# Performance work log

Hardware: AMD Instinct MI355X
Metric: run time of the kernel (lower is better)

The kernel has to match this reference:

```python
import jax, jax.numpy as jnp
import numpy as np

NUM_IN, NUM_OUT, SD, BATCH = 2048, 8192, 5, 4096
INIT_DELTA = 0.01


def _dist(a, b):
    # a: [I,1,D], b: [1,O,D] -> [I,O]
    return jnp.sqrt(jnp.sum((a - b) ** 2, axis=-1))


def setup_inputs() -> dict:
    key = jax.random.key(0)
    k1, k2, k3, k4, k5 = jax.random.split(key, 5)
    init_in_pos = jax.random.normal(k1, (NUM_IN, 1, SD), dtype=jnp.float32)
    init_out_pos = jax.random.normal(k2, (1, NUM_OUT, SD), dtype=jnp.float32)
    in_pos = init_in_pos + INIT_DELTA * jax.random.normal(k3, (NUM_IN, 1, SD), dtype=jnp.float32)
    out_pos = init_out_pos + INIT_DELTA * jax.random.normal(k4, (1, NUM_OUT, SD), dtype=jnp.float32)
    inputs = jax.random.normal(k5, (BATCH, NUM_IN), dtype=jnp.float32)
    biases = jnp.zeros((NUM_OUT,), dtype=jnp.float32)
    return {"inputs": inputs, "init_in_pos": init_in_pos, "init_out_pos": init_out_pos,
            "in_pos": in_pos, "out_pos": out_pos, "biases": biases}


def reference(inputs, init_in_pos, init_out_pos, in_pos, out_pos, biases):
    # weight = ||in_pos - out_pos|| - ||init_in_pos - init_out_pos||, shape [I,O]
    w = _dist(in_pos, out_pos) - _dist(init_in_pos, init_out_pos)
    return inputs @ w + biases
```

## Files before the change

kernel.cpp:

```cpp
#include <hip/hip_runtime.h>
#include <hip/hip_bf16.h>
#include <stdint.h>

#define NUM_IN  2048
#define NUM_OUT 8192
#define BATCH   4096
#define SD      5

#define BM 256
#define BN 256
#define BK 32
#define NT (NUM_IN / BK)
#define BUFE (BM * BK)

typedef __bf16 bf16x8 __attribute__((ext_vector_type(8)));
typedef float  f32x16 __attribute__((ext_vector_type(16)));
typedef unsigned short ushort_t;
typedef ushort_t ushort8 __attribute__((ext_vector_type(8)));

static __device__ __forceinline__ ushort_t bf16_bits(float f) {
  __hip_bfloat16 h = __float2bfloat16(f);
  ushort_t u;
  __builtin_memcpy(&u, &h, 2);
  return u;
}

__global__ __launch_bounds__(256) void cvt_kernel(const float* __restrict__ x,
                                                  ushort_t* __restrict__ y) {
  const int i = (blockIdx.x * 256 + threadIdx.x) * 8;
  float4 v0 = *reinterpret_cast<const float4*>(x + i);
  float4 v1 = *reinterpret_cast<const float4*>(x + i + 4);
  ushort8 o;
  o[0] = bf16_bits(v0.x); o[1] = bf16_bits(v0.y);
  o[2] = bf16_bits(v0.z); o[3] = bf16_bits(v0.w);
  o[4] = bf16_bits(v1.x); o[5] = bf16_bits(v1.y);
  o[6] = bf16_bits(v1.z); o[7] = bf16_bits(v1.w);
  *reinterpret_cast<ushort8*>(y + i) = o;
}

__global__ __launch_bounds__(256) void genw_kernel(
    const float* __restrict__ in_pos, const float* __restrict__ out_pos,
    const float* __restrict__ init_in, const float* __restrict__ init_out,
    ushort_t* __restrict__ Wt) {
  __shared__ float s_ip[NUM_IN * SD];
  __shared__ float s_iip[NUM_IN * SD];
  const int tid = threadIdx.x;
#pragma unroll
  for (int i = 0; i < 10; ++i) {
    const int idx = i * 1024 + tid * 4;
    *reinterpret_cast<float4*>(&s_ip[idx]) =
        *reinterpret_cast<const float4*>(in_pos + idx);
    *reinterpret_cast<float4*>(&s_iip[idx]) =
        *reinterpret_cast<const float4*>(init_in + idx);
  }
  __syncthreads();

  const int n  = blockIdx.x * 16 + (tid >> 4);
  const int kg = tid & 15;
  float op[SD], iop[SD];
#pragma unroll
  for (int d = 0; d < SD; ++d) {
    op[d]  = out_pos[n * SD + d];
    iop[d] = init_out[n * SD + d];
  }
#pragma unroll 1
  for (int kb = 0; kb < 16; ++kb) {
    const int k0 = kb * 128 + kg * 8;
    float buf[40], ibuf[40];
#pragma unroll
    for (int j = 0; j < 10; ++j) {
      float4 v = *reinterpret_cast<const float4*>(&s_ip[k0 * SD + j * 4]);
      buf[4 * j + 0] = v.x; buf[4 * j + 1] = v.y;
      buf[4 * j + 2] = v.z; buf[4 * j + 3] = v.w;
      float4 u = *reinterpret_cast<const float4*>(&s_iip[k0 * SD + j * 4]);
      ibuf[4 * j + 0] = u.x; ibuf[4 * j + 1] = u.y;
      ibuf[4 * j + 2] = u.z; ibuf[4 * j + 3] = u.w;
    }
    ushort8 o;
#pragma unroll
    for (int i = 0; i < 8; ++i) {
      float d1 = 0.f, d0 = 0.f;
#pragma unroll
      for (int d = 0; d < SD; ++d) {
        float a = buf[i * SD + d] - op[d];
        float b = ibuf[i * SD + d] - iop[d];
        d1 += a * a;
        d0 += b * b;
      }
      o[i] = bf16_bits(sqrtf(d1) - sqrtf(d0));
    }
    *reinterpret_cast<ushort8*>(Wt + (size_t)n * NUM_IN + k0) = o;
  }
}

__global__ __launch_bounds__(512, 2) void gemm_kernel(
    const ushort_t* __restrict__ A,
    const ushort_t* __restrict__ Bt,
    const float* __restrict__ bias,
    float* __restrict__ C) {
  __shared__ __align__(16) ushort_t sA[4 * BUFE];
  __shared__ __align__(16) ushort_t sB[4 * BUFE];

  const int tid = threadIdx.x;
  const int w   = tid >> 6;
  const int l   = tid & 63;
  const int wm  = w >> 2;
  const int wn  = w & 3;

  const int orig = blockIdx.x;
  const int lin  = (orig & 7) * 64 + (orig >> 3);
  const int bx   = lin >> 4;
  const int by   = lin & 15;
  const int m0   = by * BM;
  const int n0   = bx * BN;

  const int rl  = l & 31;
  const int hi  = l >> 5;
  const int le  = (l >> 1) & 7;
  const int p4  = (l & 1) * 4;
  const int phys0 = (p4 + 0 + hi) ^ le;
  const int phys1 = (p4 + 2 + hi) ^ le;
  const int lineoff = (rl >> 1) * 64;
  const int aoff0 = wm * 4096 + lineoff + phys0 * 8;
  const int aoff1 = wm * 4096 + lineoff + phys1 * 8;
  const int boff0 = wn * 2048 + lineoff + phys0 * 8;
  const int boff1 = wn * 2048 + lineoff + phys1 * 8;

  const int idx0 = tid, idx1 = tid + 512;
  const int c0 = (idx0 & 7) ^ ((idx0 >> 3) & 7);
  const int c1 = (idx1 & 7) ^ ((idx1 >> 3) & 7);
  const int row0 = 2 * (idx0 >> 3) + (c0 >> 2), k0e = (c0 & 3) * 8;
  const int row1 = 2 * (idx1 >> 3) + (c1 >> 2), k1e = (c1 & 3) * 8;
  const ushort_t* gA0 = A  + (size_t)(m0 + row0) * NUM_IN + k0e;
  const ushort_t* gA1 = A  + (size_t)(m0 + row1) * NUM_IN + k1e;
  const ushort_t* gB0 = Bt + (size_t)(n0 + row0) * NUM_IN + k0e;
  const ushort_t* gB1 = Bt + (size_t)(n0 + row1) * NUM_IN + k1e;

#define GLDS(src, dst)                                                         \
  __builtin_amdgcn_global_load_lds(                                            \
      reinterpret_cast<const __attribute__((address_space(1))) uint32_t*>(     \
          (uintptr_t)(src)),                                                   \
      reinterpret_cast<__attribute__((address_space(3))) uint32_t*>(           \
          (uintptr_t)(dst)),                                                   \
      16, 0, 0)

#define STAGE(bs, kt)                                                          \
  {                                                                            \
    GLDS(gA0 + (kt), &sA[(bs) * BUFE + idx0 * 8]);                             \
    GLDS(gA1 + (kt), &sA[(bs) * BUFE + idx1 * 8]);                             \
    GLDS(gB0 + (kt), &sB[(bs) * BUFE + idx0 * 8]);                             \
    GLDS(gB1 + (kt), &sB[(bs) * BUFE + idx1 * 8]);                             \
  }

  f32x16 acc[4][2];
#pragma unroll
  for (int i = 0; i < 4; ++i)
#pragma unroll
    for (int j = 0; j < 2; ++j)
#pragma unroll
      for (int r = 0; r < 16; ++r) acc[i][j][r] = 0.f;

  STAGE(0, 0)
  STAGE(1, BK)
  asm volatile("s_waitcnt vmcnt(4)" ::: "memory");
  __builtin_amdgcn_s_barrier();
  __builtin_amdgcn_sched_barrier(0);

#pragma unroll 1
  for (int t = 0; t < NT; ++t) {
    const int bufo = (t & 3) * BUFE;
    if (t < NT - 2) {
      STAGE((t + 2) & 3, (t + 2) * BK)
    }
    bf16x8 a[4][2], b[2][2];
#pragma unroll
    for (int mi = 0; mi < 4; ++mi) {
      a[mi][0] = *reinterpret_cast<const bf16x8*>(&sA[bufo + aoff0 + mi * 1024]);
      a[mi][1] = *reinterpret_cast<const bf16x8*>(&sA[bufo + aoff1 + mi * 1024]);
    }
#pragma unroll
    for (int ni = 0; ni < 2; ++ni) {
      b[ni][0] = *reinterpret_cast<const bf16x8*>(&sB[bufo + boff0 + ni * 1024]);
      b[ni][1] = *reinterpret_cast<const bf16x8*>(&sB[bufo + boff1 + ni * 1024]);
    }
    __builtin_amdgcn_s_setprio(1);
#pragma unroll
    for (int mi = 0; mi < 4; ++mi)
#pragma unroll
      for (int ni = 0; ni < 2; ++ni) {
        acc[mi][ni] = __builtin_amdgcn_mfma_f32_32x32x16_bf16(
            a[mi][0], b[ni][0], acc[mi][ni], 0, 0, 0);
        acc[mi][ni] = __builtin_amdgcn_mfma_f32_32x32x16_bf16(
            a[mi][1], b[ni][1], acc[mi][ni], 0, 0, 0);
      }
    __builtin_amdgcn_s_setprio(0);
    if (t < NT - 2) {
      asm volatile("s_waitcnt vmcnt(4)" ::: "memory");
    } else {
      asm volatile("s_waitcnt vmcnt(0)" ::: "memory");
    }
    __builtin_amdgcn_s_barrier();
    __builtin_amdgcn_sched_barrier(0);
  }

  const int crow = m0 + wm * 128 + 4 * hi;
  const int ccol = n0 + wn * 64 + rl;
#pragma unroll
  for (int ni = 0; ni < 2; ++ni) {
    const float bi = bias[ccol + ni * 32];
#pragma unroll
    for (int mi = 0; mi < 4; ++mi) {
#pragma unroll
      for (int reg = 0; reg < 16; ++reg) {
        const int r = crow + mi * 32 + (reg & 3) + 8 * (reg >> 2);
        C[(size_t)r * NUM_OUT + ccol + ni * 32] = acc[mi][ni][reg] + bi;
      }
    }
  }
#undef STAGE
#undef GLDS
}

extern "C" void kernel_launch(void* const* d_in, const int* in_sizes, int n_in,
                              void* d_out, int out_size, void* d_ws, size_t ws_size,
                              hipStream_t stream) {
  const float* inputs   = (const float*)d_in[0];
  const float* init_in  = (const float*)d_in[1];
  const float* init_out = (const float*)d_in[2];
  const float* in_pos   = (const float*)d_in[3];
  const float* out_pos  = (const float*)d_in[4];
  const float* biases   = (const float*)d_in[5];
  float* out = (float*)d_out;

  ushort_t* Abf = (ushort_t*)d_ws;
  ushort_t* Wt  = (ushort_t*)((char*)d_ws + (size_t)BATCH * NUM_IN * 2);

  cvt_kernel<<<(BATCH * NUM_IN) / (256 * 8), 256, 0, stream>>>(inputs, Abf);
  genw_kernel<<<NUM_OUT / 16, 256, 0, stream>>>(
      in_pos, out_pos, init_in, init_out, Wt);
  gemm_kernel<<<(BATCH / BM) * (NUM_OUT / BN), 512, 0, stream>>>(
      Abf, Wt, biases, out);
}
```

Baseline: 185.3 us.

## Restructure GEMM into 8-phase ping-pong schedule with 16x16x32 MFMA and BK=64

Measured after the change: 165.8 us. 10.5% less time.

```diff
diff --git a/kernel.cpp b/kernel.cpp
--- a/kernel.cpp
+++ b/kernel.cpp
@@ -9,12 +9,13 @@
 
 #define BM 256
 #define BN 256
-#define BK 32
+#define BK 64
 #define NT (NUM_IN / BK)
-#define BUFE (BM * BK)
+#define NI (NT / 2)
+#define TILEE (BM * BK)
 
 typedef __bf16 bf16x8 __attribute__((ext_vector_type(8)));
-typedef float  f32x16 __attribute__((ext_vector_type(16)));
+typedef float  f32x4  __attribute__((ext_vector_type(4)));
 typedef unsigned short ushort_t;
 typedef ushort_t ushort8 __attribute__((ext_vector_type(8)));
 
@@ -93,19 +94,21 @@
   }
 }
 
-__global__ __launch_bounds__(512, 2) void gemm_kernel(
+__global__ __launch_bounds__(512, 1) void gemm_kernel(
     const ushort_t* __restrict__ A,
     const ushort_t* __restrict__ Bt,
     const float* __restrict__ bias,
     float* __restrict__ C) {
-  __shared__ __align__(16) ushort_t sA[4 * BUFE];
-  __shared__ __align__(16) ushort_t sB[4 * BUFE];
-
-  const int tid = threadIdx.x;
-  const int w   = tid >> 6;
-  const int l   = tid & 63;
-  const int wm  = w >> 2;
-  const int wn  = w & 3;
+  __shared__ __align__(16) ushort_t sA[2 * TILEE];
+  __shared__ __align__(16) ushort_t sB[2 * TILEE];
+
+  const int tid  = threadIdx.x;
+  const int w    = tid >> 6;
+  const int l    = tid & 63;
+  const int wm   = w >> 2;
+  const int wn   = w & 3;
+  const int lrow = l & 15;
+  const int lkc  = l >> 4;
 
   const int orig = blockIdx.x;
   const int lin  = (orig & 7) * 64 + (orig >> 3);
@@ -114,27 +117,19 @@
   const int m0   = by * BM;
   const int n0   = bx * BN;
 
-  const int rl  = l & 31;
-  const int hi  = l >> 5;
-  const int le  = (l >> 1) & 7;
-  const int p4  = (l & 1) * 4;
-  const int phys0 = (p4 + 0 + hi) ^ le;
-  const int phys1 = (p4 + 2 + hi) ^ le;
-  const int lineoff = (rl >> 1) * 64;
-  const int aoff0 = wm * 4096 + lineoff + phys0 * 8;
-  const int aoff1 = wm * 4096 + lineoff + phys1 * 8;
-  const int boff0 = wn * 2048 + lineoff + phys0 * 8;
-  const int boff1 = wn * 2048 + lineoff + phys1 * 8;
-
-  const int idx0 = tid, idx1 = tid + 512;
-  const int c0 = (idx0 & 7) ^ ((idx0 >> 3) & 7);
-  const int c1 = (idx1 & 7) ^ ((idx1 >> 3) & 7);
-  const int row0 = 2 * (idx0 >> 3) + (c0 >> 2), k0e = (c0 & 3) * 8;
-  const int row1 = 2 * (idx1 >> 3) + (c1 >> 2), k1e = (c1 & 3) * 8;
-  const ushort_t* gA0 = A  + (size_t)(m0 + row0) * NUM_IN + k0e;
-  const ushort_t* gA1 = A  + (size_t)(m0 + row1) * NUM_IN + k1e;
-  const ushort_t* gB0 = Bt + (size_t)(n0 + row0) * NUM_IN + k0e;
-  const ushort_t* gB1 = Bt + (size_t)(n0 + row1) * NUM_IN + k1e;
+  const int ck0 = (lkc ^ (lrow & 7)) * 8;
+  const int ck1 = ((4 + lkc) ^ (lrow & 7)) * 8;
+  const int Ab  = wm * 4096 + lrow * 64;
+  const int Bb  = wn * 2048 + lrow * 64;
+
+  const int d0 = tid, d1 = tid + 512;
+  const int lr0 = d0 >> 3, lr1 = d1 >> 3;
+  const int c0 = (d0 & 7) ^ (lr0 & 7);
+  const int c1 = (d1 & 7) ^ (lr1 & 7);
+  const ushort_t* pA0 = A  + (size_t)(m0 + (lr0 >> 6) * 128 + (lr0 & 63)) * NUM_IN + c0 * 8;
+  const ushort_t* pA1 = A  + (size_t)(m0 + (lr1 >> 6) * 128 + (lr1 & 63)) * NUM_IN + c1 * 8;
+  const ushort_t* pB0 = Bt + (size_t)(n0 + (lr0 >> 5) * 64 + (lr0 & 31)) * NUM_IN + c0 * 8;
+  const ushort_t* pB1 = Bt + (size_t)(n0 + (lr1 >> 5) * 64 + (lr1 & 31)) * NUM_IN + c1 * 8;
 
 #define GLDS(src, dst)                                                         \
   __builtin_amdgcn_global_load_lds(                                            \
@@ -144,80 +139,162 @@
           (uintptr_t)(dst)),                                                   \
       16, 0, 0)
 
-#define STAGE(bs, kt)                                                          \
-  {                                                                            \
-    GLDS(gA0 + (kt), &sA[(bs) * BUFE + idx0 * 8]);                             \
-    GLDS(gA1 + (kt), &sA[(bs) * BUFE + idx1 * 8]);                             \
-    GLDS(gB0 + (kt), &sB[(bs) * BUFE + idx0 * 8]);                             \
-    GLDS(gB1 + (kt), &sB[(bs) * BUFE + idx1 * 8]);                             \
-  }
-
-  f32x16 acc[4][2];
-#pragma unroll
-  for (int i = 0; i < 4; ++i)
-#pragma unroll
-    for (int j = 0; j < 2; ++j)
-#pragma unroll
-      for (int r = 0; r < 16; ++r) acc[i][j][r] = 0.f;
-
-  STAGE(0, 0)
-  STAGE(1, BK)
-  asm volatile("s_waitcnt vmcnt(4)" ::: "memory");
-  __builtin_amdgcn_s_barrier();
-  __builtin_amdgcn_sched_barrier(0);
+#define STAGE_A(bs, mh, kt)                                                    \
+  {                                                                            \
+    GLDS(pA0 + (size_t)(mh) * 64 * NUM_IN + (kt),                              \
+         &sA[(bs) * TILEE + (mh) * 8192 + tid * 8]);                           \
+    GLDS(pA1 + (size_t)(mh) * 64 * NUM_IN + (kt),                              \
+         &sA[(bs) * TILEE + (mh) * 8192 + tid * 8 + 4096]);                    \
+  }
+#define STAGE_B(bs, nh, kt)                                                    \
+  {                                                                            \
+    GLDS(pB0 + (size_t)(nh) * 32 * NUM_IN + (kt),                              \
+         &sB[(bs) * TILEE + (nh) * 8192 + tid * 8]);                           \
+    GLDS(pB1 + (size_t)(nh) * 32 * NUM_IN + (kt),                              \
+         &sB[(bs) * TILEE + (nh) * 8192 + tid * 8 + 4096]);                    \
+  }
+
+#define RD_A(bs, mh)                                                           \
+  {                                                                            \
+    _Pragma("unroll")                                                          \
+    for (int mi = 0; mi < 4; ++mi) {                                           \
+      a[mi][0] = *reinterpret_cast<const bf16x8*>(                             \
+          &sA[(bs) * TILEE + (mh) * 8192 + Ab + mi * 1024 + ck0]);             \
+      a[mi][1] = *reinterpret_cast<const bf16x8*>(                             \
+          &sA[(bs) * TILEE + (mh) * 8192 + Ab + mi * 1024 + ck1]);             \
+    }                                                                          \
+  }
+#define RD_B(bs, nh, arr)                                                      \
+  {                                                                            \
+    _Pragma("unroll")                                                          \
+    for (int nj = 0; nj < 2; ++nj) {                                           \
+      arr[nj][0] = *reinterpret_cast<const bf16x8*>(                           \
+          &sB[(bs) * TILEE + (nh) * 8192 + Bb + nj * 1024 + ck0]);             \
+      arr[nj][1] = *reinterpret_cast<const bf16x8*>(                           \
+          &sB[(bs) * TILEE + (nh) * 8192 + Bb + nj * 1024 + ck1]);             \
+    }                                                                          \
+  }
+
+#define MFMA_Q(mh, nh, arr)                                                    \
+  {                                                                            \
+    __builtin_amdgcn_s_setprio(1);                                             \
+    _Pragma("unroll")                                                          \
+    for (int mi = 0; mi < 4; ++mi)                                             \
+      _Pragma("unroll")                                                        \
+      for (int nj = 0; nj < 2; ++nj) {                                         \
+        acc[(mh) * 4 + mi][(nh) * 2 + nj] =                                    \
+            __builtin_amdgcn_mfma_f32_16x16x32_bf16(                           \
+                a[mi][0], arr[nj][0], acc[(mh) * 4 + mi][(nh) * 2 + nj],       \
+                0, 0, 0);                                                      \
+        acc[(mh) * 4 + mi][(nh) * 2 + nj] =                                    \
+            __builtin_amdgcn_mfma_f32_16x16x32_bf16(                           \
+                a[mi][1], arr[nj][1], acc[(mh) * 4 + mi][(nh) * 2 + nj],       \
+                0, 0, 0);                                                      \
+      }                                                                        \
+    __builtin_amdgcn_s_setprio(0);                                             \
+  }
+
+#define BARRIER  __builtin_amdgcn_s_barrier()
+#define SCHED0   __builtin_amdgcn_sched_barrier(0)
+#define LGKM0    asm volatile("s_waitcnt lgkmcnt(0)" ::: "memory")
+#define VMCNT4   asm volatile("s_waitcnt vmcnt(4)" ::: "memory")
+
+  f32x4 acc[8][4];
+#pragma unroll
+  for (int i = 0; i < 8; ++i)
+#pragma unroll
+    for (int j = 0; j < 4; ++j) acc[i][j] = f32x4{0.f, 0.f, 0.f, 0.f};
+
+  STAGE_A(0, 0, 0) STAGE_B(0, 0, 0) STAGE_A(0, 1, 0) STAGE_B(0, 1, 0)
+  STAGE_A(1, 0, BK) STAGE_B(1, 0, BK)
+  VMCNT4;
+  BARRIER;
+  SCHED0;
 
 #pragma unroll 1
-  for (int t = 0; t < NT; ++t) {
-    const int bufo = (t & 3) * BUFE;
-    if (t < NT - 2) {
-      STAGE((t + 2) & 3, (t + 2) * BK)
-    }
-    bf16x8 a[4][2], b[2][2];
-#pragma unroll
-    for (int mi = 0; mi < 4; ++mi) {
-      a[mi][0] = *reinterpret_cast<const bf16x8*>(&sA[bufo + aoff0 + mi * 1024]);
-      a[mi][1] = *reinterpret_cast<const bf16x8*>(&sA[bufo + aoff1 + mi * 1024]);
-    }
-#pragma unroll
-    for (int ni = 0; ni < 2; ++ni) {
-      b[ni][0] = *reinterpret_cast<const bf16x8*>(&sB[bufo + boff0 + ni * 1024]);
-      b[ni][1] = *reinterpret_cast<const bf16x8*>(&sB[bufo + boff1 + ni * 1024]);
-    }
-    __builtin_amdgcn_s_setprio(1);
-#pragma unroll
-    for (int mi = 0; mi < 4; ++mi)
-#pragma unroll
-      for (int ni = 0; ni < 2; ++ni) {
-        acc[mi][ni] = __builtin_amdgcn_mfma_f32_32x32x16_bf16(
-            a[mi][0], b[ni][0], acc[mi][ni], 0, 0, 0);
-        acc[mi][ni] = __builtin_amdgcn_mfma_f32_32x32x16_bf16(
-            a[mi][1], b[ni][1], acc[mi][ni], 0, 0, 0);
-      }
-    __builtin_amdgcn_s_setprio(0);
-    if (t < NT - 2) {
-      asm volatile("s_waitcnt vmcnt(4)" ::: "memory");
-    } else {
-      asm volatile("s_waitcnt vmcnt(0)" ::: "memory");
-    }
-    __builtin_amdgcn_s_barrier();
-    __builtin_amdgcn_sched_barrier(0);
-  }
-
-  const int crow = m0 + wm * 128 + 4 * hi;
-  const int ccol = n0 + wn * 64 + rl;
-#pragma unroll
-  for (int ni = 0; ni < 2; ++ni) {
-    const float bi = bias[ccol + ni * 32];
-#pragma unroll
-    for (int mi = 0; mi < 4; ++mi) {
-#pragma unroll
-      for (int reg = 0; reg < 16; ++reg) {
-        const int r = crow + mi * 32 + (reg & 3) + 8 * (reg >> 2);
-        C[(size_t)r * NUM_OUT + ccol + ni * 32] = acc[mi][ni][reg] + bi;
+  for (int it = 0; it < NI; ++it) {
+    const int t1k = (2 * it + 1) * BK;
+    const int t2  = 2 * it + 2, t3 = 2 * it + 3;
+    const int t2k = (t2 < NT ? t2 : NT - 1) * BK;
+    const int t3k = (t3 < NT ? t3 : NT - 1) * BK;
+    bf16x8 a[4][2], b0[2][2], b1[2][2];
+
+    RD_A(0, 0) RD_B(0, 0, b0)
+    STAGE_A(1, 1, t1k)
+    BARRIER; LGKM0; SCHED0;
+    MFMA_Q(0, 0, b0)
+    BARRIER; SCHED0;
+
+    RD_B(0, 1, b1)
+    STAGE_B(1, 1, t1k)
+    BARRIER; LGKM0; SCHED0;
+    MFMA_Q(0, 1, b1)
+    BARRIER; SCHED0;
+
+    RD_A(0, 1)
+    STAGE_A(0, 0, t2k)
+    BARRIER; LGKM0; SCHED0;
+    MFMA_Q(1, 0, b0)
+    BARRIER; SCHED0;
+
+    STAGE_B(0, 0, t2k)
+    BARRIER; SCHED0;
+    MFMA_Q(1, 1, b1)
+    VMCNT4;
+    BARRIER; SCHED0;
+
+    RD_A(1, 0) RD_B(1, 0, b0)
+    STAGE_A(0, 1, t2k)
+    BARRIER; LGKM0; SCHED0;
+    MFMA_Q(0, 0, b0)
+    BARRIER; SCHED0;
+
+    RD_B(1, 1, b1)
+    STAGE_B(0, 1, t2k)
+    BARRIER; LGKM0; SCHED0;
+    MFMA_Q(0, 1, b1)
+    BARRIER; SCHED0;
+
+    RD_A(1, 1)
+    STAGE_A(1, 0, t3k)
+    BARRIER; LGKM0; SCHED0;
+    MFMA_Q(1, 0, b0)
+    BARRIER; SCHED0;
+
+    STAGE_B(1, 0, t3k)
+    BARRIER; SCHED0;
+    MFMA_Q(1, 1, b1)
+    VMCNT4;
+    BARRIER; SCHED0;
+  }
+
+  const int er = l >> 4;
+  const int ec = l & 15;
+#pragma unroll
+  for (int nh = 0; nh < 2; ++nh) {
+#pragma unroll
+    for (int nj = 0; nj < 2; ++nj) {
+      const int col = n0 + wn * 64 + nh * 32 + nj * 16 + ec;
+      const float bi = bias[col];
+#pragma unroll
+      for (int mh = 0; mh < 2; ++mh) {
+#pragma unroll
+        for (int mi = 0; mi < 4; ++mi) {
+#pragma unroll
+          for (int j = 0; j < 4; ++j) {
+            const int row = m0 + wm * 128 + mh * 64 + mi * 16 + er * 4 + j;
+            C[(size_t)row * NUM_OUT + col] =
+                acc[mh * 4 + mi][nh * 2 + nj][j] + bi;
+          }
+        }
       }
     }
   }
-#undef STAGE
+#undef STAGE_A
+#undef STAGE_B
+#undef RD_A
+#undef RD_B
+#undef MFMA_Q
 #undef GLDS
 }
 
```
